# Optimization experiments

Hardware: AMD Instinct MI355X
Metric: run time of the kernel (lower is better)

Reference implementation:

```python
import jax, jax.numpy as jnp
import numpy as np

RAY_DIR = jnp.array([0.4395064455, 0.617598629942, 0.652231566745], dtype=jnp.float32)
TOL = 1e-7
CONTACT_THRESH = 25.0   # opt.contact_thresh
COLLISION_THRESH = 25.0  # opt.collision_thresh
BIG = 1e10


def mesh_contains(points, triangles, tri_valid):
    """Moller-Trumbore ray casting (fixed ray dir), parity test.
    points [B,P,3], triangles [B,T,3,3], tri_valid [B,T] -> exterior [B,P] bool."""
    v0, v1, v2 = triangles[:, :, 0, :], triangles[:, :, 1, :], triangles[:, :, 2, :]
    e1 = v1 - v0
    e2 = v2 - v0
    pvec = jnp.cross(jnp.broadcast_to(RAY_DIR, e2.shape), e2)          # [B,T,3]
    dets = jnp.sum(e1 * pvec, -1)                                      # [B,T]
    parallel = jnp.abs(dets) < TOL
    invdet = 1.0 / (dets + 0.1 * TOL)
    tvec = points[:, None, :, :] - v0[:, :, None, :]                   # [B,T,P,3]
    u = jnp.sum(tvec * pvec[:, :, None, :], -1) * invdet[:, :, None]   # [B,T,P]
    qvec = jnp.cross(tvec, e1[:, :, None, :])                          # [B,T,P,3]
    v = jnp.sum(qvec * RAY_DIR, -1) * invdet[:, :, None]
    t = jnp.sum(e2[:, :, None, :] * qvec, -1) * invdet[:, :, None]
    inter = (u > 0) & (u < 1) & (v > 0) & (u + v < 1) & (t > TOL)
    inter = inter & (~parallel & tri_valid)[:, :, None]
    n_hits = jnp.sum(inter.astype(jnp.int32), axis=1)                  # [B,P]
    return (n_hits % 2) == 0


def masked_mean_loss(vals, mask):
    m = mask.astype(vals.dtype)
    tot = m.sum()
    loss = jnp.where(tot > 0, (m * vals).sum() / jnp.maximum(tot, 1.0), 0.0)
    row = m.sum(1)
    losses = jnp.where(row > 0, (m * vals).sum(1) / jnp.maximum(row, 1.0), 0.0)
    return loss, losses


def setup_inputs() -> dict:
    key = jax.random.key(0)
    ks = jax.random.split(key, 6)
    B, Nh, Fh, No, Fo = 8, 778, 1538, 2000, 4000
    hand_verts = jax.random.normal(ks[0], (B, Nh, 3), dtype=jnp.float32)
    hand_faces = jax.random.randint(ks[1], (B, Fh, 3), 0, Nh, dtype=jnp.int32)
    obj_verts = jax.random.normal(ks[2], (B, No, 3), dtype=jnp.float32)
    obj_faces = jax.random.randint(ks[3], (B, Fo, 3), 0, 1200, dtype=jnp.int32)
    obj_vert_splits = 1200 + jax.random.randint(ks[4], (B,), 0, No - 1200 + 1, dtype=jnp.int32)
    obj_face_splits = 2400 + jax.random.randint(ks[5], (B,), 0, Fo - 2400 + 1, dtype=jnp.int32)
    return {"hand_verts": hand_verts, "hand_faces": hand_faces,
            "obj_verts": obj_verts, "obj_faces": obj_faces,
            "obj_vert_splits": obj_vert_splits, "obj_face_splits": obj_face_splits}


def reference(hand_verts, hand_faces, obj_verts, obj_faces, obj_vert_splits, obj_face_splits):
    B, Nh, _ = hand_verts.shape
    No = obj_verts.shape[1]
    Fo = obj_faces.shape[1]
    sg = jax.lax.stop_gradient

    # gather triangles (batched)
    hand_tri = jax.vmap(lambda v, f: v[f])(hand_verts, hand_faces)     # [B,Fh,3,3]
    obj_tri = jax.vmap(lambda v, f: v[f])(obj_verts, obj_faces)        # [B,Fo,3,3]

    face_valid = jnp.arange(Fo)[None, :] < obj_face_splits[:, None]    # [B,Fo]
    vert_valid = jnp.arange(No)[None, :] < obj_vert_splits[:, None]    # [B,No]

    # containment tests run on detached geometry (as in original)
    hand_tri_valid = jnp.ones(hand_tri.shape[:2], dtype=bool)
    exterior_obj = mesh_contains(sg(obj_verts), sg(hand_tri), hand_tri_valid)   # [B,No]
    exterior_hand = mesh_contains(sg(hand_verts), sg(obj_tri), face_valid)      # [B,Nh]

    penetr_o_mask = (~exterior_obj) & vert_valid
    penetr_h_mask = ~exterior_hand

    # ragged squared pairwise distances (bmm form of original), padded cols -> BIG
    rx = jnp.sum(hand_verts * hand_verts, -1)                          # [B,Nh]
    ry = jnp.sum(obj_verts * obj_verts, -1)                            # [B,No]
    zz = jnp.einsum('bnd,bmd->bnm', hand_verts, obj_verts)             # [B,Nh,No]
    dists = rx[:, :, None] + ry[:, None, :] - 2.0 * zz
    dists = jnp.where(vert_valid[:, None, :], dists, BIG)

    minoh_idxs = jnp.argmin(dists, axis=1)                             # [B,No]
    minho_idxs = jnp.argmin(dists, axis=2)                             # [B,Nh]

    results_close = jnp.take_along_axis(obj_verts, minho_idxs[:, :, None], axis=1)    # [B,Nh,3]
    results_o_close = jnp.take_along_axis(hand_verts, minoh_idxs[:, :, None], axis=1)  # [B,No,3]

    # contact_target == 'all'
    anchor_dists = jnp.sqrt(jnp.sum((results_close - hand_verts) ** 2, -1))    # [B,Nh]
    anchor_o_dist = jnp.sqrt(jnp.sum((results_o_close - obj_verts) ** 2, -1))  # [B,No]

    # contact_mode == 'dist_tanh' -> below_dist all ones
    contact_vals = CONTACT_THRESH * jnp.tanh(anchor_dists / CONTACT_THRESH)
    # collision_mode == 'dist_tanh'
    collision_vals = COLLISION_THRESH * jnp.tanh(anchor_dists / COLLISION_THRESH)
    collision_o_vals = COLLISION_THRESH * jnp.tanh(anchor_o_dist / COLLISION_THRESH)
    collision_o_vals = jnp.where(vert_valid, collision_o_vals, 0.0)

    # contact_zones == 'all'
    missed_mask = exterior_hand

    missed_loss, missed_losses = masked_mean_loss(contact_vals, missed_mask)
    penetr_h_loss, penetr_h_losses = masked_mean_loss(collision_vals, penetr_h_mask)
    penetr_o_loss, penetr_o_losses = masked_mean_loss(collision_o_vals, penetr_o_mask)
    penetr_loss = penetr_h_loss + penetr_o_loss
    penetr_losses = penetr_h_losses + penetr_o_losses

    return missed_loss, penetr_loss, missed_losses, penetr_losses
```

## Files before the change

kernel.cpp:

```cpp
#include <hip/hip_runtime.h>


#define RX 0.4395064455f
#define RY 0.617598629942f
#define RZ 0.652231566745f

#define MAXCHUNK_F4 512
#define PTS_PER_BLK 512

struct Params {
    const float* hand_verts; const int* hand_faces;
    const float* obj_verts;  const int* obj_faces;
    const int* ovsplit; const int* ofsplit;
    int* hitsA;
    int* hitsB;
    float* anchor_h; float* anchor_o;
    float* partials;
    unsigned int* done;
    float* out;
    int B, Nh, Fh, No, Fo;
    int pbA, CA, chunkA, blocksA;
    int pbB, CB, chunkB, blocksB;
};

__device__ __forceinline__ void tri_pre_one(const float* __restrict__ vb,
                                            const int* __restrict__ f,
                                            float4* o) {
#pragma clang fp contract(off)
    int i0 = f[0], i1 = f[1], i2 = f[2];
    float v0x = vb[i0*3+0], v0y = vb[i0*3+1], v0z = vb[i0*3+2];
    float v1x = vb[i1*3+0], v1y = vb[i1*3+1], v1z = vb[i1*3+2];
    float v2x = vb[i2*3+0], v2y = vb[i2*3+1], v2z = vb[i2*3+2];
    float e1x = v1x - v0x, e1y = v1y - v0y, e1z = v1z - v0z;
    float e2x = v2x - v0x, e2y = v2y - v0y, e2z = v2z - v0z;
    float px = RY*e2z - RZ*e2y;
    float py = RZ*e2x - RX*e2z;
    float pz = RX*e2y - RY*e2x;
    float det = (e1x*px + e1y*py) + e1z*pz;
    float invdet = 1.0f / (det + 1e-8f);
    bool valid = !(fabsf(det) < 1e-7f);
    o[0] = make_float4(v0x, v0y, v0z, invdet);
    o[1] = make_float4(e1x, e1y, e1z, valid ? 1.0f : 0.0f);
    o[2] = make_float4(e2x, e2y, e2z, 0.0f);
    o[3] = make_float4(px,  py,  pz,  0.0f);
}

__device__ __forceinline__ int mt_test(float qx, float qy, float qz,
                                       const float4& f0, const float4& f1,
                                       const float4& f2, const float4& f3) {
#pragma clang fp contract(off)
    float tvx = qx - f0.x, tvy = qy - f0.y, tvz = qz - f0.z;
    float u  = ((tvx*f3.x + tvy*f3.y) + tvz*f3.z) * f0.w;
    float qvx = tvy*f1.z - tvz*f1.y;
    float qvy = tvz*f1.x - tvx*f1.z;
    float qvz = tvx*f1.y - tvy*f1.x;
    float v  = ((qvx*RX + qvy*RY) + qvz*RZ) * f0.w;
    float tt = ((f2.x*qvx + f2.y*qvy) + f2.z*qvz) * f0.w;
    bool hit = (u > 0.0f) && (u < 1.0f) && (v > 0.0f) &&
               ((u + v) < 1.0f) && (tt > 1e-7f) && (f1.w != 0.0f);
    return hit ? 1 : 0;
}

__device__ __forceinline__ void raycast_vb(const Params& p, int vbid, int tid,
                                           float4* s_tri) {
#pragma clang fp contract(off)
    const float* pts; const float* tverts; const int* tfaces; int* slots;
    int P, T, Nv, c, pb, b, chunk, tlim, plim;
    if (vbid < p.blocksA) {
        int per_b = p.pbA * p.CA;
        b  = vbid / per_b;
        int r = vbid - b * per_b;
        c  = r / p.pbA;
        pb = r - c * p.pbA;
        pts = p.obj_verts; tverts = p.hand_verts; tfaces = p.hand_faces;
        slots = p.hitsA;
        P = p.No; T = p.Fh; Nv = p.Nh; chunk = p.chunkA;
        tlim = p.Fh; plim = min(p.No, p.ovsplit[b]);
    } else {
        int j = vbid - p.blocksA;
        int per_b = p.pbB * p.CB;
        b  = j / per_b;
        int r = j - b * per_b;
        c  = r / p.pbB;
        pb = r - c * p.pbB;
        pts = p.hand_verts; tverts = p.obj_verts; tfaces = p.obj_faces;
        slots = p.hitsB;
        P = p.Nh; T = p.Fo; Nv = p.No; chunk = p.chunkB;
        tlim = min(p.Fo, p.ofsplit[b]); plim = p.Nh;
    }

    int tStart = c * chunk;
    if (tStart >= tlim) return;
    if (pb * PTS_PER_BLK >= plim) return;
    int nTri = min(tStart + chunk, tlim) - tStart;

    if (tid < nTri) {
        int t = tStart + tid;
        tri_pre_one(tverts + (size_t)b * Nv * 3,
                    tfaces + ((size_t)b * T + t) * 3,
                    s_tri + (size_t)tid * 4);
    }

    int p1 = pb * PTS_PER_BLK + tid;
    int p2 = p1 + 256;
    bool act1 = p1 < plim, act2 = p2 < plim;
    float q1x = 0.f, q1y = 0.f, q1z = 0.f;
    float q2x = 0.f, q2y = 0.f, q2z = 0.f;
    if (act1) {
        const float* q = pts + ((size_t)b * P + p1) * 3;
        q1x = q[0]; q1y = q[1]; q1z = q[2];
    }
    if (act2) {
        const float* q = pts + ((size_t)b * P + p2) * 3;
        q2x = q[0]; q2y = q[1]; q2z = q[2];
    }
    __syncthreads();

    if (!act1) return;
    int cnt1 = 0, cnt2 = 0;
    for (int i = 0; i < nTri; ++i) {
        const float4 f0 = s_tri[(i<<2)+0];
        const float4 f1 = s_tri[(i<<2)+1];
        const float4 f2 = s_tri[(i<<2)+2];
        const float4 f3 = s_tri[(i<<2)+3];
        cnt1 += mt_test(q1x, q1y, q1z, f0, f1, f2, f3);
        cnt2 += mt_test(q2x, q2y, q2z, f0, f1, f2, f3);
    }
    int* base = slots + ((size_t)(c * p.B + b)) * P;
    base[p1] = cnt1;
    if (act2) base[p2] = cnt2;
}

__device__ __forceinline__ void min_one(const Params& p, int w, int lane) {
#pragma clang fp contract(off)
    int nHand = p.B * p.Nh;
    const float* refv; const float* loopv; int loopN; float* outp;
    if (w < nHand) {
        int b = w / p.Nh;
        int n = w - b * p.Nh;
        refv  = p.hand_verts + ((size_t)b * p.Nh + n) * 3;
        loopv = p.obj_verts + (size_t)b * p.No * 3;
        loopN = p.ovsplit[b];
        outp  = p.anchor_h + (size_t)b * p.Nh + n;
    } else {
        int j = w - nHand;
        int b = j / p.No;
        int m = j - b * p.No;
        if (m >= p.ovsplit[b]) return;
        refv  = p.obj_verts + ((size_t)b * p.No + m) * 3;
        loopv = p.hand_verts + (size_t)b * p.Nh * 3;
        loopN = p.Nh;
        outp  = p.anchor_o + (size_t)b * p.No + m;
    }
    float hx = refv[0], hy = refv[1], hz = refv[2];
    float rx = (hx*hx + hy*hy) + hz*hz;
    unsigned long long best = ~0ull;
    for (int m = lane; m < loopN; m += 64) {
        float ox = loopv[m*3+0], oy = loopv[m*3+1], oz = loopv[m*3+2];
        float ry = (ox*ox + oy*oy) + oz*oz;
        float zz = (hx*ox + hy*oy) + hz*oz;
        float d = (rx + ry) - 2.0f * zz;
        unsigned long long e = ((unsigned long long)__float_as_uint(d) << 32) | (unsigned)m;
        if (e < best) best = e;
    }
    for (int off = 32; off > 0; off >>= 1) {
        unsigned long long o = __shfl_xor(best, off, 64);
        if (o < best) best = o;
    }
    if (lane == 0) {
        int idx = (best == ~0ull) ? 0 : (int)(best & 0xffffffffu);
        const float* cv = loopv + (size_t)idx * 3;
        float dx = cv[0] - hx, dy = cv[1] - hy, dz = cv[2] - hz;
        *outp = sqrtf((dx*dx + dy*dy) + dz*dz);
    }
}

__global__ __launch_bounds__(256) void mega(Params p) {
    __shared__ float4 s_tri[MAXCHUNK_F4];
    const int tid = threadIdx.x;
    const int bid = blockIdx.x;
    if (bid == 0 && tid == 0) *p.done = 0u;
    const int nRay = p.blocksA + p.blocksB;
    if (bid < nRay) {
        raycast_vb(p, bid, tid, s_tri);
    } else {
        int w = (bid - nRay) * 4 + (tid >> 6);
        if (w < p.B * (p.Nh + p.No)) min_one(p, w, tid & 63);
    }
}

__global__ __launch_bounds__(64) void reduce_fin(Params p) {
    const int r    = blockIdx.x;
    const int b    = r >> 4;
    const int wv   = r & 15;
    const int lane = threadIdx.x;
    const int vt   = wv * 64 + lane;
    float s0=0.f,s1=0.f,s2=0.f,s3=0.f,s4=0.f,s5=0.f;

    int tlimB = min(p.Fo, p.ofsplit[b]);
    int nCB = (tlimB + p.chunkB - 1) / p.chunkB;
    for (int n = vt; n < p.Nh; n += 1024) {
        int par = 0;
        for (int c = 0; c < nCB; ++c)
            par += p.hitsB[((size_t)(c * p.B + b)) * p.Nh + n];
        bool ext = (par & 1) == 0;
        float val = 25.0f * tanhf(p.anchor_h[(size_t)b*p.Nh + n] / 25.0f);
        if (ext) { s0 += val; s1 += 1.0f; } else { s2 += val; s3 += 1.0f; }
    }
    int split = p.ovsplit[b];
    for (int m = vt; m < split; m += 1024) {
        int par = 0;
        for (int c = 0; c < p.CA; ++c)
            par += p.hitsA[((size_t)(c * p.B + b)) * p.No + m];
        if (par & 1) {
            s4 += 25.0f * tanhf(p.anchor_o[(size_t)b*p.No + m] / 25.0f);
            s5 += 1.0f;
        }
    }
    for (int off = 32; off > 0; off >>= 1) {
        s0 += __shfl_xor(s0, off, 64);
        s1 += __shfl_xor(s1, off, 64);
        s2 += __shfl_xor(s2, off, 64);
        s3 += __shfl_xor(s3, off, 64);
        s4 += __shfl_xor(s4, off, 64);
        s5 += __shfl_xor(s5, off, 64);
    }

    __shared__ bool s_last;
    if (lane == 0) {
        float* q = p.partials + ((size_t)(b * 16 + wv)) * 6;
        q[0]=s0; q[1]=s1; q[2]=s2; q[3]=s3; q[4]=s4; q[5]=s5;
        __threadfence();
        unsigned int old = atomicAdd(p.done, 1u);
        s_last = (old == (unsigned int)(gridDim.x - 1));
    }
    __syncthreads();
    if (!s_last) return;
    __threadfence();

    __shared__ float s_red[16][6];
    if (lane < p.B && lane < 16) {
        int bb = lane;
        float t0=0.f,t1=0.f,t2=0.f,t3=0.f,t4=0.f,t5=0.f;
        for (int w2 = 0; w2 < 16; ++w2) {
            const float* q = p.partials + ((size_t)(bb * 16 + w2)) * 6;
            t0 += q[0]; t1 += q[1]; t2 += q[2];
            t3 += q[3]; t4 += q[4]; t5 += q[5];
        }
        p.out[2 + bb]  = (t1 > 0.f) ? t0 / fmaxf(t1, 1.f) : 0.f;
        float ph       = (t3 > 0.f) ? t2 / fmaxf(t3, 1.f) : 0.f;
        float po       = (t5 > 0.f) ? t4 / fmaxf(t5, 1.f) : 0.f;
        p.out[10 + bb] = ph + po;
        s_red[bb][0]=t0; s_red[bb][1]=t1; s_red[bb][2]=t2;
        s_red[bb][3]=t3; s_red[bb][4]=t4; s_red[bb][5]=t5;
    }
    __syncthreads();
    if (lane == 0) {
        float sm=0.f,cm=0.f,sph=0.f,cph=0.f,spo=0.f,cpo=0.f;
        for (int bb = 0; bb < p.B; ++bb) {
            sm  += s_red[bb][0]; cm  += s_red[bb][1]; sph += s_red[bb][2];
            cph += s_red[bb][3]; spo += s_red[bb][4]; cpo += s_red[bb][5];
        }
        float missed = (cm  > 0.f) ? sm  / fmaxf(cm , 1.f) : 0.f;
        float ph     = (cph > 0.f) ? sph / fmaxf(cph, 1.f) : 0.f;
        float po     = (cpo > 0.f) ? spo / fmaxf(cpo, 1.f) : 0.f;
        p.out[0] = missed;
        p.out[1] = ph + po;
    }
}

extern "C" void kernel_launch(void* const* d_in, const int* in_sizes, int n_in,
                              void* d_out, int out_size, void* d_ws, size_t ws_size,
                              hipStream_t stream) {
    Params p;
    p.hand_verts = (const float*)d_in[0];
    p.hand_faces = (const int*)d_in[1];
    p.obj_verts  = (const float*)d_in[2];
    p.obj_faces  = (const int*)d_in[3];
    p.ovsplit    = (const int*)d_in[4];
    p.ofsplit    = (const int*)d_in[5];
    p.out        = (float*)d_out;

    p.B  = in_sizes[4];
    p.Nh = in_sizes[0] / (3 * p.B);
    p.Fh = in_sizes[1] / (3 * p.B);
    p.No = in_sizes[2] / (3 * p.B);
    p.Fo = in_sizes[3] / (3 * p.B);

    p.CA = 16; p.CB = 32;
    p.chunkA = (p.Fh + p.CA - 1) / p.CA;
    p.chunkB = (p.Fo + p.CB - 1) / p.CB;
    p.pbA = (p.No + PTS_PER_BLK - 1) / PTS_PER_BLK;
    p.pbB = (p.Nh + PTS_PER_BLK - 1) / PTS_PER_BLK;
    p.blocksA = p.pbA * p.CA * p.B;
    p.blocksB = p.pbB * p.CB * p.B;

    char* ws = (char*)d_ws;
    size_t off = 0;
    auto alloc = [&](size_t bytes) -> void* {
        void* q = ws + off;
        off = (off + bytes + 255) & ~(size_t)255;
        return q;
    };
    p.hitsA    = (int*)   alloc((size_t)p.CA * p.B * p.No * sizeof(int));
    p.hitsB    = (int*)   alloc((size_t)p.CB * p.B * p.Nh * sizeof(int));
    p.anchor_h = (float*) alloc((size_t)p.B * p.Nh * sizeof(float));
    p.anchor_o = (float*) alloc((size_t)p.B * p.No * sizeof(float));
    p.partials = (float*) alloc((size_t)p.B * 16 * 6 * sizeof(float));
    p.done     = (unsigned int*)alloc(sizeof(unsigned int));

    int totalMin   = p.B * (p.Nh + p.No);
    int nMinBlocks = (totalMin + 3) / 4;
    int grid = p.blocksA + p.blocksB + nMinBlocks;

    mega<<<grid, 256, 0, stream>>>(p);
    reduce_fin<<<p.B * 16, 64, 0, stream>>>(p);
}
```

Before: 132.9 us.

## Restructure raycast to wave-level tasks with triangles in lanes and ballot counting

Raycasting is now split into per-wavefront tasks instead of 256-thread blocks. Each lane holds one triangle in registers, and query points are broadcast through readlane. Per-point hit counts come from ballot plus popcount, which removes the shared-memory triangle staging and the block syncs. Because triangle ranges are only 64 wide, the partial hit arrays grow, so reduce_fin has more slots to sum per point, and each point iteration carries extra ballot and readlane overhead.

After: 177.2 us. +33.3%, slower.

```diff
diff --git a/kernel.cpp b/kernel.cpp
--- a/kernel.cpp
+++ b/kernel.cpp
@@ -5,8 +5,7 @@
 #define RY 0.617598629942f
 #define RZ 0.652231566745f
 
-#define MAXCHUNK_F4 512
-#define PTS_PER_BLK 512
+#define PTS_PER_TASK 128
 
 struct Params {
     const float* hand_verts; const int* hand_faces;
@@ -19,14 +18,40 @@
     unsigned int* done;
     float* out;
     int B, Nh, Fh, No, Fo;
-    int pbA, CA, chunkA, blocksA;
-    int pbB, CB, chunkB, blocksB;
+    int nRangeA, nPSA, taskA;
+    int nRangeB, nPSB, taskB;
+    int nRayW;
 };
 
-__device__ __forceinline__ void tri_pre_one(const float* __restrict__ vb,
-                                            const int* __restrict__ f,
-                                            float4* o) {
+__device__ __forceinline__ void raycast_wave(const Params& p, int w, int lane) {
 #pragma clang fp contract(off)
+    const float* pts; const float* tverts; const int* tfaces; int* slots;
+    int P, T, Nv, b, r, ps, tlim, plim;
+    if (w < p.taskA) {
+        int perB = p.nRangeA * p.nPSA;
+        b = w / perB; int rem = w - b * perB;
+        r = rem / p.nPSA; ps = rem - r * p.nPSA;
+        pts = p.obj_verts; tverts = p.hand_verts; tfaces = p.hand_faces;
+        slots = p.hitsA; P = p.No; T = p.Fh; Nv = p.Nh;
+        tlim = p.Fh; plim = min(p.No, p.ovsplit[b]);
+    } else {
+        int j = w - p.taskA;
+        int perB = p.nRangeB * p.nPSB;
+        b = j / perB; int rem = j - b * perB;
+        r = rem / p.nPSB; ps = rem - r * p.nPSB;
+        pts = p.hand_verts; tverts = p.obj_verts; tfaces = p.obj_faces;
+        slots = p.hitsB; P = p.Nh; T = p.Fo; Nv = p.No;
+        tlim = min(p.Fo, p.ofsplit[b]); plim = p.Nh;
+    }
+
+    int pBase = ps * PTS_PER_TASK;
+    if (pBase >= plim) return;
+    if (r * 64 >= tlim) return;
+
+    int t  = r * 64 + lane;
+    int tc = min(t, tlim - 1);
+    const int* f = tfaces + ((size_t)b * T + tc) * 3;
+    const float* vb = tverts + (size_t)b * Nv * 3;
     int i0 = f[0], i1 = f[1], i2 = f[2];
     float v0x = vb[i0*3+0], v0y = vb[i0*3+1], v0z = vb[i0*3+2];
     float v1x = vb[i1*3+0], v1y = vb[i1*3+1], v1z = vb[i1*3+2];
@@ -38,97 +63,56 @@
     float pz = RX*e2y - RY*e2x;
     float det = (e1x*px + e1y*py) + e1z*pz;
     float invdet = 1.0f / (det + 1e-8f);
-    bool valid = !(fabsf(det) < 1e-7f);
-    o[0] = make_float4(v0x, v0y, v0z, invdet);
-    o[1] = make_float4(e1x, e1y, e1z, valid ? 1.0f : 0.0f);
-    o[2] = make_float4(e2x, e2y, e2z, 0.0f);
-    o[3] = make_float4(px,  py,  pz,  0.0f);
-}
-
-__device__ __forceinline__ int mt_test(float qx, float qy, float qz,
-                                       const float4& f0, const float4& f1,
-                                       const float4& f2, const float4& f3) {
-#pragma clang fp contract(off)
-    float tvx = qx - f0.x, tvy = qy - f0.y, tvz = qz - f0.z;
-    float u  = ((tvx*f3.x + tvy*f3.y) + tvz*f3.z) * f0.w;
-    float qvx = tvy*f1.z - tvz*f1.y;
-    float qvy = tvz*f1.x - tvx*f1.z;
-    float qvz = tvx*f1.y - tvy*f1.x;
-    float v  = ((qvx*RX + qvy*RY) + qvz*RZ) * f0.w;
-    float tt = ((f2.x*qvx + f2.y*qvy) + f2.z*qvz) * f0.w;
-    bool hit = (u > 0.0f) && (u < 1.0f) && (v > 0.0f) &&
-               ((u + v) < 1.0f) && (tt > 1e-7f) && (f1.w != 0.0f);
-    return hit ? 1 : 0;
-}
-
-__device__ __forceinline__ void raycast_vb(const Params& p, int vbid, int tid,
-                                           float4* s_tri) {
-#pragma clang fp contract(off)
-    const float* pts; const float* tverts; const int* tfaces; int* slots;
-    int P, T, Nv, c, pb, b, chunk, tlim, plim;
-    if (vbid < p.blocksA) {
-        int per_b = p.pbA * p.CA;
-        b  = vbid / per_b;
-        int r = vbid - b * per_b;
-        c  = r / p.pbA;
-        pb = r - c * p.pbA;
-        pts = p.obj_verts; tverts = p.hand_verts; tfaces = p.hand_faces;
-        slots = p.hitsA;
-        P = p.No; T = p.Fh; Nv = p.Nh; chunk = p.chunkA;
-        tlim = p.Fh; plim = min(p.No, p.ovsplit[b]);
-    } else {
-        int j = vbid - p.blocksA;
-        int per_b = p.pbB * p.CB;
-        b  = j / per_b;
-        int r = j - b * per_b;
-        c  = r / p.pbB;
-        pb = r - c * p.pbB;
-        pts = p.hand_verts; tverts = p.obj_verts; tfaces = p.obj_faces;
-        slots = p.hitsB;
-        P = p.Nh; T = p.Fo; Nv = p.No; chunk = p.chunkB;
-        tlim = min(p.Fo, p.ofsplit[b]); plim = p.Nh;
-    }
-
-    int tStart = c * chunk;
-    if (tStart >= tlim) return;
-    if (pb * PTS_PER_BLK >= plim) return;
-    int nTri = min(tStart + chunk, tlim) - tStart;
-
-    if (tid < nTri) {
-        int t = tStart + tid;
-        tri_pre_one(tverts + (size_t)b * Nv * 3,
-                    tfaces + ((size_t)b * T + t) * 3,
-                    s_tri + (size_t)tid * 4);
-    }
-
-    int p1 = pb * PTS_PER_BLK + tid;
-    int p2 = p1 + 256;
-    bool act1 = p1 < plim, act2 = p2 < plim;
-    float q1x = 0.f, q1y = 0.f, q1z = 0.f;
-    float q2x = 0.f, q2y = 0.f, q2z = 0.f;
-    if (act1) {
-        const float* q = pts + ((size_t)b * P + p1) * 3;
-        q1x = q[0]; q1y = q[1]; q1z = q[2];
-    }
-    if (act2) {
-        const float* q = pts + ((size_t)b * P + p2) * 3;
-        q2x = q[0]; q2y = q[1]; q2z = q[2];
-    }
-    __syncthreads();
-
-    if (!act1) return;
-    int cnt1 = 0, cnt2 = 0;
-    for (int i = 0; i < nTri; ++i) {
-        const float4 f0 = s_tri[(i<<2)+0];
-        const float4 f1 = s_tri[(i<<2)+1];
-        const float4 f2 = s_tri[(i<<2)+2];
-        const float4 f3 = s_tri[(i<<2)+3];
-        cnt1 += mt_test(q1x, q1y, q1z, f0, f1, f2, f3);
-        cnt2 += mt_test(q2x, q2y, q2z, f0, f1, f2, f3);
-    }
-    int* base = slots + ((size_t)(c * p.B + b)) * P;
-    base[p1] = cnt1;
-    if (act2) base[p2] = cnt2;
+    if (t >= tlim || fabsf(det) < 1e-7f) invdet = 0.0f;
+
+    int p0 = pBase + lane, p1 = p0 + 64;
+    bool a0 = p0 < plim, a1 = p1 < plim;
+    int pc0 = min(p0, plim - 1), pc1 = min(p1, plim - 1);
+    const float* q0 = pts + ((size_t)b * P + pc0) * 3;
+    const float* q1 = pts + ((size_t)b * P + pc1) * 3;
+    float q0x = q0[0], q0y = q0[1], q0z = q0[2];
+    float q1x = q1[0], q1y = q1[1], q1z = q1[2];
+
+    int live0 = min(plim - pBase, 64);
+    int live1 = min(max(plim - pBase - 64, 0), 64);
+    int cnt0 = 0, cnt1 = 0;
+
+    for (int j = 0; j < live0; ++j) {
+        float qx = __int_as_float(__builtin_amdgcn_readlane(__float_as_int(q0x), j));
+        float qy = __int_as_float(__builtin_amdgcn_readlane(__float_as_int(q0y), j));
+        float qz = __int_as_float(__builtin_amdgcn_readlane(__float_as_int(q0z), j));
+        float tvx = qx - v0x, tvy = qy - v0y, tvz = qz - v0z;
+        float u  = ((tvx*px + tvy*py) + tvz*pz) * invdet;
+        float qvx = tvy*e1z - tvz*e1y;
+        float qvy = tvz*e1x - tvx*e1z;
+        float qvz = tvx*e1y - tvy*e1x;
+        float v  = ((qvx*RX + qvy*RY) + qvz*RZ) * invdet;
+        float tt = ((e2x*qvx + e2y*qvy) + e2z*qvz) * invdet;
+        bool hit = (u > 0.0f) && (u < 1.0f) && (v > 0.0f) &&
+                   ((u + v) < 1.0f) && (tt > 1e-7f);
+        int pc = __popcll(__ballot(hit));
+        cnt0 = (lane == j) ? pc : cnt0;
+    }
+    for (int j = 0; j < live1; ++j) {
+        float qx = __int_as_float(__builtin_amdgcn_readlane(__float_as_int(q1x), j));
+        float qy = __int_as_float(__builtin_amdgcn_readlane(__float_as_int(q1y), j));
+        float qz = __int_as_float(__builtin_amdgcn_readlane(__float_as_int(q1z), j));
+        float tvx = qx - v0x, tvy = qy - v0y, tvz = qz - v0z;
+        float u  = ((tvx*px + tvy*py) + tvz*pz) * invdet;
+        float qvx = tvy*e1z - tvz*e1y;
+        float qvy = tvz*e1x - tvx*e1z;
+        float qvz = tvx*e1y - tvy*e1x;
+        float v  = ((qvx*RX + qvy*RY) + qvz*RZ) * invdet;
+        float tt = ((e2x*qvx + e2y*qvy) + e2z*qvz) * invdet;
+        bool hit = (u > 0.0f) && (u < 1.0f) && (v > 0.0f) &&
+                   ((u + v) < 1.0f) && (tt > 1e-7f);
+        int pc = __popcll(__ballot(hit));
+        cnt1 = (lane == j) ? pc : cnt1;
+    }
+
+    int* base = slots + ((size_t)(r * p.B + b)) * P;
+    if (a0) base[p0] = cnt0;
+    if (a1) base[p1] = cnt1;
 }
 
 __device__ __forceinline__ void min_one(const Params& p, int w, int lane) {
@@ -176,16 +160,16 @@
 }
 
 __global__ __launch_bounds__(256) void mega(Params p) {
-    __shared__ float4 s_tri[MAXCHUNK_F4];
     const int tid = threadIdx.x;
     const int bid = blockIdx.x;
     if (bid == 0 && tid == 0) *p.done = 0u;
-    const int nRay = p.blocksA + p.blocksB;
-    if (bid < nRay) {
-        raycast_vb(p, bid, tid, s_tri);
+    int w = bid * 4 + (tid >> 6);
+    int lane = tid & 63;
+    if (w < p.nRayW) {
+        raycast_wave(p, w, lane);
     } else {
-        int w = (bid - nRay) * 4 + (tid >> 6);
-        if (w < p.B * (p.Nh + p.No)) min_one(p, w, tid & 63);
+        int mw = w - p.nRayW;
+        if (mw < p.B * (p.Nh + p.No)) min_one(p, mw, lane);
     }
 }
 
@@ -198,7 +182,7 @@
     float s0=0.f,s1=0.f,s2=0.f,s3=0.f,s4=0.f,s5=0.f;
 
     int tlimB = min(p.Fo, p.ofsplit[b]);
-    int nCB = (tlimB + p.chunkB - 1) / p.chunkB;
+    int nCB = (tlimB + 63) >> 6;
     for (int n = vt; n < p.Nh; n += 1024) {
         int par = 0;
         for (int c = 0; c < nCB; ++c)
@@ -210,7 +194,7 @@
     int split = p.ovsplit[b];
     for (int m = vt; m < split; m += 1024) {
         int par = 0;
-        for (int c = 0; c < p.CA; ++c)
+        for (int c = 0; c < p.nRangeA; ++c)
             par += p.hitsA[((size_t)(c * p.B + b)) * p.No + m];
         if (par & 1) {
             s4 += 25.0f * tanhf(p.anchor_o[(size_t)b*p.No + m] / 25.0f);
@@ -287,13 +271,13 @@
     p.No = in_sizes[2] / (3 * p.B);
     p.Fo = in_sizes[3] / (3 * p.B);
 
-    p.CA = 16; p.CB = 32;
-    p.chunkA = (p.Fh + p.CA - 1) / p.CA;
-    p.chunkB = (p.Fo + p.CB - 1) / p.CB;
-    p.pbA = (p.No + PTS_PER_BLK - 1) / PTS_PER_BLK;
-    p.pbB = (p.Nh + PTS_PER_BLK - 1) / PTS_PER_BLK;
-    p.blocksA = p.pbA * p.CA * p.B;
-    p.blocksB = p.pbB * p.CB * p.B;
+    p.nRangeA = (p.Fh + 63) / 64;
+    p.nRangeB = (p.Fo + 63) / 64;
+    p.nPSA = (p.No + PTS_PER_TASK - 1) / PTS_PER_TASK;
+    p.nPSB = (p.Nh + PTS_PER_TASK - 1) / PTS_PER_TASK;
+    p.taskA = p.B * p.nRangeA * p.nPSA;
+    p.taskB = p.B * p.nRangeB * p.nPSB;
+    p.nRayW = p.taskA + p.taskB;
 
     char* ws = (char*)d_ws;
     size_t off = 0;
@@ -302,16 +286,16 @@
         off = (off + bytes + 255) & ~(size_t)255;
         return q;
     };
-    p.hitsA    = (int*)   alloc((size_t)p.CA * p.B * p.No * sizeof(int));
-    p.hitsB    = (int*)   alloc((size_t)p.CB * p.B * p.Nh * sizeof(int));
+    p.hitsA    = (int*)   alloc((size_t)p.nRangeA * p.B * p.No * sizeof(int));
+    p.hitsB    = (int*)   alloc((size_t)p.nRangeB * p.B * p.Nh * sizeof(int));
     p.anchor_h = (float*) alloc((size_t)p.B * p.Nh * sizeof(float));
     p.anchor_o = (float*) alloc((size_t)p.B * p.No * sizeof(float));
     p.partials = (float*) alloc((size_t)p.B * 16 * 6 * sizeof(float));
     p.done     = (unsigned int*)alloc(sizeof(unsigned int));
 
-    int totalMin   = p.B * (p.Nh + p.No);
-    int nMinBlocks = (totalMin + 3) / 4;
-    int grid = p.blocksA + p.blocksB + nMinBlocks;
+    int totalMin = p.B * (p.Nh + p.No);
+    int totalW   = p.nRayW + totalMin;
+    int grid     = (totalW + 3) / 4;
 
     mega<<<grid, 256, 0, stream>>>(p);
     reduce_fin<<<p.B * 16, 64, 0, stream>>>(p);
```
